# Kernel tuning notes

Measured on AMD Instinct MI355X. Metric: run time of the kernel, lower is better.

## Reference

```python
import jax, jax.numpy as jnp
import numpy as np

B, S, H = 128, 512, 768      # batch, seq, encoder hidden
NL = 42                      # len(LABEL_TO_ID)
LD = 300                     # label_dim
DK, DV = 64, 768             # K_dim, V_dim
HID = 768                    # opt['hidden_dim']
P = 512                      # max_seq_length == pos_indicator
INF = 1e12                   # constant.INFINITY_NUMBER
NEG = -1e9


def gelu(x):
    return 0.5 * x * (1.0 + jax.lax.erf(x * 0.7071067811865476))


def setup_inputs() -> dict:
    key = jax.random.key(0)
    ks = jax.random.split(key, 24)
    sc = 0.02
    return {
        "inputs": jax.random.normal(ks[0], (B, S, H), jnp.float32),
        "pos_ids": jax.random.randint(ks[1], (B, S), 0, 53),
        "dep_ids": jax.random.randint(ks[2], (B, S), 0, 42),
        "subj_pos": jax.random.randint(ks[3], (B, S), 0, P + 1),
        "obj_pos": jax.random.randint(ks[4], (B, S), 0, P + 1),
        "adj": jnp.zeros((1, 1, 1), jnp.float32),  # unused by forward
        # stacked per-label Q/K projections (41 = NL-1 labels, label 0 excluded)
        "WQ": jax.random.normal(ks[5], (NL - 1, DK, H), jnp.float32) * sc,
        "bQ": jax.random.normal(ks[6], (NL - 1, DK), jnp.float32) * sc,
        "WK": jax.random.normal(ks[7], (NL - 1, DK, LD), jnp.float32) * sc,
        "bK": jax.random.normal(ks[8], (NL - 1, DK), jnp.float32) * sc,
        "WV_w": jax.random.normal(ks[9], (DV, H), jnp.float32) * sc,
        "WV_b": jax.random.normal(ks[10], (DV,), jnp.float32) * sc,
        "Wout_w": jax.random.normal(ks[11], (H, DV), jnp.float32) * sc,
        "Wout_b": jax.random.normal(ks[12], (H,), jnp.float32) * sc,
        "ln_g": jnp.ones((H,), jnp.float32),
        "ln_b": jnp.zeros((H,), jnp.float32),
        "label_emb": jax.random.normal(ks[13], (NL, LD), jnp.float32) * sc,
        "feat_w": jax.random.normal(ks[14], (HID, 3 * H), jnp.float32) * sc,
        "feat_b": jax.random.normal(ks[15], (HID,), jnp.float32) * sc,
        "out_w": jax.random.normal(ks[16], (LD, HID), jnp.float32) * sc,
        "out_b": jax.random.normal(ks[17], (LD,), jnp.float32) * sc,
    }


def reference(inputs, pos_ids, dep_ids, subj_pos, obj_pos, adj,
              WQ, bQ, WK, bK, WV_w, WV_b, Wout_w, Wout_b, ln_g, ln_b,
              label_emb, feat_w, feat_b, out_w, out_b):
    dt = inputs.dtype
    # combined attention mask (bool OR, as torch bool+bool): entity markers + padding
    mask = (subj_pos == P) | (obj_pos == P) | (pos_ids == 0)   # [B,S]

    # --- LabelAttention: 41-loop collapses to one fused projection ---
    lab = label_emb[1:NL]                                      # [41,LD] labels 1..41
    kvec = jnp.einsum('ld,lkd->lk', lab, WK) + bK              # [41,DK] per-label keys
    # scores_sum[b,s] = sum_l (x W_Q_l^T + b_Q_l) . k_l  /sqrt(dk)  + 41*mask*NEG
    w_eff = jnp.einsum('lk,lkh->h', kvec, WQ)                  # [H]
    c = jnp.sum(kvec * bQ)                                     # scalar
    scores = (inputs @ w_eff + c) / 8.0                        # sqrt(DK)=8; [B,S]
    scores = scores + (NL - 1) * mask.astype(dt) * NEG
    attn = jax.nn.softmax(scores, axis=-1)                     # [B,S]

    wv = inputs @ WV_w.T + WV_b                                # [B,S,DV]
    ctx = jnp.einsum('bs,bsd->bd', attn, wv)                   # [B,DV]
    ctx = gelu(ctx @ Wout_w.T + Wout_b)                        # [B,H]
    mu = ctx.mean(-1, keepdims=True)
    var = ((ctx - mu) ** 2).mean(-1, keepdims=True)
    ctx = (ctx - mu) / jnp.sqrt(var + 1e-5) * ln_g + ln_b

    # --- entity max pooling (mask True where NOT part of entity) ---
    sm = (subj_pos != P)[:, :, None]
    om = (obj_pos != P)[:, :, None]
    subj_out = jnp.where(sm, -INF, inputs).max(axis=1)         # [B,H]
    obj_out = jnp.where(om, -INF, inputs).max(axis=1)          # [B,H]

    feats = jnp.concatenate([subj_out, obj_out, ctx], axis=-1)  # [B,3H]
    feats = gelu(feats @ feat_w.T + feat_b)                     # [B,HID]
    feats = gelu(feats @ out_w.T + out_b)                       # [B,LD]

    logits = feats @ label_emb.T                                # [B,42]
    return logits, ctx
```

## Files before the change

kernel.cpp:

```cpp
#include <hip/hip_runtime.h>
#include <math.h>

#define BB 128
#define SS 512
#define HH 768
#define PPOS 512
#define NEGC (-1.0e9f)
#define NINF (-1.0e12f)

#define OFF_KVEC   0
#define OFF_WEFF   2624
#define OFF_C      3392
#define OFF_CAT    0
#define OFF_POOLED 294912
#define OFF_PP     393216
#define OFF_PS     1179648
#define OFF_PO     1966080
#define OFF_PZ     2752512
#define OFF_CTXA   393216
#define OFF_CTXB   491520
#define OFF_F1     589824
#define OFF_F2     688128

__device__ __forceinline__ float gelu_f(float x) {
    return 0.5f * x * (1.0f + erff(x * 0.70710678118654752f));
}
__device__ __forceinline__ float dot4(float4 a, float4 b) {
    return a.x*b.x + a.y*b.y + a.z*b.z + a.w*b.w;
}

template<int K4, int ACT, int MT>
__global__ __launch_bounds__(256) void k_mm(const float* __restrict__ A,
        const float* __restrict__ W, const float* __restrict__ bias,
        float* __restrict__ C, int M, int N) {
    int lane = threadIdx.x & 63;
    int wave = (blockIdx.x * 256 + threadIdx.x) >> 6;
    int ntn = (N + 15) >> 4;
    int m0 = (wave / ntn) * MT;
    if (m0 >= M) return;
    int n0 = ((wave % ntn) << 4) + (lane >> 2);
    int ks = lane & 3;
    bool nvalid = (n0 < N);
    const float4* A4 = (const float4*)A;
    const float4* w_row = (const float4*)W + (size_t)(nvalid ? n0 : 0) * K4;
    const float4* ar = A4 + (size_t)m0 * K4;
    float acc[MT];
    #pragma unroll
    for (int r = 0; r < MT; ++r) acc[r] = 0.f;
    #pragma unroll 4
    for (int j = ks; j < K4; j += 4) {
        float4 wv = w_row[j];
        #pragma unroll
        for (int r = 0; r < MT; ++r) acc[r] += dot4(ar[(size_t)r * K4 + j], wv);
    }
    #pragma unroll
    for (int r = 0; r < MT; ++r) {
        acc[r] += __shfl_xor(acc[r], 1, 64);
        acc[r] += __shfl_xor(acc[r], 2, 64);
    }
    if (ks == 0 && nvalid) {
        float b = bias ? bias[n0] : 0.f;
        #pragma unroll
        for (int r = 0; r < MT; ++r) {
            float v = acc[r] + b;
            if (ACT == 1) v = gelu_f(v);
            C[(size_t)(m0 + r) * N + n0] = v;
        }
    }
}

__global__ __launch_bounds__(256) void k_kvec2(const float* __restrict__ label_emb,
        const float* __restrict__ WK, const float* __restrict__ bK,
        float* __restrict__ ws) {
    if (blockIdx.x < 3) ws[OFF_WEFF + blockIdx.x * 256 + threadIdx.x] = 0.f;
    if (blockIdx.x == 3 && threadIdx.x == 0) ws[OFF_C] = 0.f;
    int lane = threadIdx.x & 63;
    int idx = (blockIdx.x * 256 + threadIdx.x) >> 6;
    int l = idx >> 6;
    const float4* lab4 = (const float4*)(label_emb + (size_t)(l + 1) * 300);
    const float4* wk4  = (const float4*)(WK + (size_t)idx * 300);
    float acc = dot4(lab4[lane], wk4[lane]);
    if (lane < 11) acc += dot4(lab4[64 + lane], wk4[64 + lane]);
    #pragma unroll
    for (int off = 32; off > 0; off >>= 1) acc += __shfl_xor(acc, off, 64);
    if (lane == 0) ws[OFF_KVEC + idx] = acc + bK[idx];
}

__global__ __launch_bounds__(256) void k_weff2(const float* __restrict__ WQ,
        const float* __restrict__ bQ, float* __restrict__ ws) {
    int lane = threadIdx.x & 63;
    int w = (blockIdx.x * 256 + threadIdx.x) >> 6;
    if (w < 492) {
        int jc = w / 12, hg = w % 12;
        int h = hg * 64 + lane;
        const float* wq = WQ + (size_t)(jc * 64) * HH + h;
        const float* kv = ws + OFF_KVEC + jc * 64;
        float acc = 0.f;
        #pragma unroll 8
        for (int j = 0; j < 64; ++j) acc += kv[j] * wq[(size_t)j * HH];
        atomicAdd(&ws[OFF_WEFF + h], acc);
    } else if (w == 492) {
        float acc = 0.f;
        for (int j = lane; j < 2624; j += 64) acc += ws[OFF_KVEC + j] * bQ[j];
        #pragma unroll
        for (int off = 32; off > 0; off >>= 1) acc += __shfl_xor(acc, off, 64);
        if (lane == 0) atomicAdd(&ws[OFF_C], acc);
    }
}

__global__ __launch_bounds__(256) void k_fused(const float* __restrict__ inputs,
        const int* __restrict__ pos_ids, const int* __restrict__ subj_pos,
        const int* __restrict__ obj_pos, float* __restrict__ ws) {
    __shared__ float l_pe[4][768];
    __shared__ float l_sm[4][768];
    __shared__ float l_om[4][768];
    __shared__ float l_z[4];
    __shared__ int l_mask[64];
    int chunk = blockIdx.x, b = blockIdx.y;
    int t = threadIdx.x, wave = t >> 6, lane = t & 63;
    int row0 = b * SS + chunk * 64;
    if (t < 64) {
        int g = row0 + t;
        int sp = subj_pos[g], op = obj_pos[g], pi = pos_ids[g];
        int m = ((sp == PPOS) | (op == PPOS) | (pi == 0)) ? 1 : 0;
        if (sp == PPOS) m |= 2;
        if (op == PPOS) m |= 4;
        l_mask[t] = m;
    }
    const float4* w4 = (const float4*)(ws + OFF_WEFF);
    float c = ws[OFF_C];
    float4 w0 = w4[lane], w1 = w4[64 + lane], w2 = w4[128 + lane];
    __syncthreads();
    const float4* in4 = (const float4*)inputs;
    float4 pe0 = make_float4(0.f, 0.f, 0.f, 0.f);
    float4 pe1 = pe0, pe2 = pe0;
    float4 sm0 = make_float4(NINF, NINF, NINF, NINF);
    float4 sm1 = sm0, sm2 = sm0, om0 = sm0, om1 = sm0, om2 = sm0;
    float z = 0.f;
    int rbase = wave * 16;
    #pragma unroll 4
    for (int r = 0; r < 16; ++r) {
        int s = rbase + r;
        const float4* x4 = in4 + (size_t)(row0 + s) * 192;
        float4 x0 = x4[lane], x1 = x4[64 + lane], x2 = x4[128 + lane];
        float acc = dot4(x0, w0) + dot4(x1, w1) + dot4(x2, w2);
        #pragma unroll
        for (int off = 32; off > 0; off >>= 1) acc += __shfl_xor(acc, off, 64);
        int mk = l_mask[s];
        float e = (mk & 1) ? 0.f : __expf((acc + c) * 0.125f);
        z += e;
        pe0.x += e * x0.x; pe0.y += e * x0.y; pe0.z += e * x0.z; pe0.w += e * x0.w;
        pe1.x += e * x1.x; pe1.y += e * x1.y; pe1.z += e * x1.z; pe1.w += e * x1.w;
        pe2.x += e * x2.x; pe2.y += e * x2.y; pe2.z += e * x2.z; pe2.w += e * x2.w;
        if (mk & 2) {
            sm0.x = fmaxf(sm0.x, x0.x); sm0.y = fmaxf(sm0.y, x0.y);
            sm0.z = fmaxf(sm0.z, x0.z); sm0.w = fmaxf(sm0.w, x0.w);
            sm1.x = fmaxf(sm1.x, x1.x); sm1.y = fmaxf(sm1.y, x1.y);
            sm1.z = fmaxf(sm1.z, x1.z); sm1.w = fmaxf(sm1.w, x1.w);
            sm2.x = fmaxf(sm2.x, x2.x); sm2.y = fmaxf(sm2.y, x2.y);
            sm2.z = fmaxf(sm2.z, x2.z); sm2.w = fmaxf(sm2.w, x2.w);
        }
        if (mk & 4) {
            om0.x = fmaxf(om0.x, x0.x); om0.y = fmaxf(om0.y, x0.y);
            om0.z = fmaxf(om0.z, x0.z); om0.w = fmaxf(om0.w, x0.w);
            om1.x = fmaxf(om1.x, x1.x); om1.y = fmaxf(om1.y, x1.y);
            om1.z = fmaxf(om1.z, x1.z); om1.w = fmaxf(om1.w, x1.w);
            om2.x = fmaxf(om2.x, x2.x); om2.y = fmaxf(om2.y, x2.y);
            om2.z = fmaxf(om2.z, x2.z); om2.w = fmaxf(om2.w, x2.w);
        }
    }
    ((float4*)l_pe[wave])[lane] = pe0;
    ((float4*)l_pe[wave])[64 + lane] = pe1;
    ((float4*)l_pe[wave])[128 + lane] = pe2;
    ((float4*)l_sm[wave])[lane] = sm0;
    ((float4*)l_sm[wave])[64 + lane] = sm1;
    ((float4*)l_sm[wave])[128 + lane] = sm2;
    ((float4*)l_om[wave])[lane] = om0;
    ((float4*)l_om[wave])[64 + lane] = om1;
    ((float4*)l_om[wave])[128 + lane] = om2;
    if (lane == 0) l_z[wave] = z;
    __syncthreads();
    if (t < 192) {
        float4 p = make_float4(0.f, 0.f, 0.f, 0.f);
        float4 s = make_float4(NINF, NINF, NINF, NINF);
        float4 o = s;
        #pragma unroll
        for (int w = 0; w < 4; ++w) {
            float4 vp = ((float4*)l_pe[w])[t];
            float4 vs = ((float4*)l_sm[w])[t];
            float4 vo = ((float4*)l_om[w])[t];
            p.x += vp.x; p.y += vp.y; p.z += vp.z; p.w += vp.w;
            s.x = fmaxf(s.x, vs.x); s.y = fmaxf(s.y, vs.y);
            s.z = fmaxf(s.z, vs.z); s.w = fmaxf(s.w, vs.w);
            o.x = fmaxf(o.x, vo.x); o.y = fmaxf(o.y, vo.y);
            o.z = fmaxf(o.z, vo.z); o.w = fmaxf(o.w, vo.w);
        }
        size_t oo = (size_t)(b * 8 + chunk) * 192 + t;
        ((float4*)(ws + OFF_PP))[oo] = p;
        ((float4*)(ws + OFF_PS))[oo] = s;
        ((float4*)(ws + OFF_PO))[oo] = o;
    }
    if (t == 0) ws[OFF_PZ + b * 8 + chunk] = l_z[0] + l_z[1] + l_z[2] + l_z[3];
}

__global__ void k_reduce(float* __restrict__ ws) {
    int i = blockIdx.x * 256 + threadIdx.x;
    int b = i / HH, h = i - b * HH;
    float p = 0.f, sm = NINF, om = NINF, zt = 0.f;
    #pragma unroll
    for (int j = 0; j < 8; ++j) {
        int o = (b * 8 + j) * HH + h;
        p += ws[OFF_PP + o];
        sm = fmaxf(sm, ws[OFF_PS + o]);
        om = fmaxf(om, ws[OFF_PO + o]);
        zt += ws[OFF_PZ + b * 8 + j];
    }
    ws[OFF_POOLED + i] = p / zt;
    ws[OFF_CAT + (size_t)b * 2304 + h] = sm;
    ws[OFF_CAT + (size_t)b * 2304 + 768 + h] = om;
}

__global__ void k_ln(const float* __restrict__ ln_g, const float* __restrict__ ln_b,
                     float* __restrict__ ws, float* __restrict__ out) {
    __shared__ float red[256];
    __shared__ float red2[256];
    int b = blockIdx.x, t = threadIdx.x;
    const float* x = ws + OFF_CTXB + (size_t)b * HH;
    float a0 = x[t], a1 = x[t + 256], a2 = x[t + 512];
    red[t]  = a0 + a1 + a2;
    red2[t] = a0 * a0 + a1 * a1 + a2 * a2;
    __syncthreads();
    for (int s2 = 128; s2 > 0; s2 >>= 1) {
        if (t < s2) { red[t] += red[t + s2]; red2[t] += red2[t + s2]; }
        __syncthreads();
    }
    float mu  = red[0] * (1.0f / 768.0f);
    float var = red2[0] * (1.0f / 768.0f) - mu * mu;
    float inv = rsqrtf(var + 1e-5f);
    float* o = out + 5376 + (size_t)b * HH;
    float* cc = ws + OFF_CAT + (size_t)b * 2304 + 1536;
    float r0 = (a0 - mu) * inv * ln_g[t]       + ln_b[t];
    float r1 = (a1 - mu) * inv * ln_g[t + 256] + ln_b[t + 256];
    float r2 = (a2 - mu) * inv * ln_g[t + 512] + ln_b[t + 512];
    o[t] = r0; o[t + 256] = r1; o[t + 512] = r2;
    cc[t] = r0; cc[t + 256] = r1; cc[t + 512] = r2;
}

extern "C" void kernel_launch(void* const* d_in, const int* in_sizes, int n_in,
                              void* d_out, int out_size, void* d_ws, size_t ws_size,
                              hipStream_t stream) {
    const float* inputs    = (const float*)d_in[0];
    const int*   pos_ids   = (const int*)d_in[1];
    const int*   subj_pos  = (const int*)d_in[3];
    const int*   obj_pos   = (const int*)d_in[4];
    const float* WQ        = (const float*)d_in[6];
    const float* bQ        = (const float*)d_in[7];
    const float* WK        = (const float*)d_in[8];
    const float* bK        = (const float*)d_in[9];
    const float* WV_w      = (const float*)d_in[10];
    const float* WV_b      = (const float*)d_in[11];
    const float* Wout_w    = (const float*)d_in[12];
    const float* Wout_b    = (const float*)d_in[13];
    const float* ln_g      = (const float*)d_in[14];
    const float* ln_b      = (const float*)d_in[15];
    const float* label_emb = (const float*)d_in[16];
    const float* feat_w    = (const float*)d_in[17];
    const float* feat_b    = (const float*)d_in[18];
    const float* out_w     = (const float*)d_in[19];
    const float* out_b     = (const float*)d_in[20];
    float* out = (float*)d_out;
    float* ws  = (float*)d_ws;

    k_kvec2  <<<656, 256, 0, stream>>>(label_emb, WK, bK, ws);
    k_weff2  <<<124, 256, 0, stream>>>(WQ, bQ, ws);
    k_fused  <<<dim3(8, BB), 256, 0, stream>>>(inputs, pos_ids, subj_pos, obj_pos, ws);
    k_reduce <<<384, 256, 0, stream>>>(ws);
    k_mm<192,0,2><<<768, 256, 0, stream>>>(ws + OFF_POOLED, WV_w, WV_b, ws + OFF_CTXA, BB, HH);
    k_mm<192,1,2><<<768, 256, 0, stream>>>(ws + OFF_CTXA, Wout_w, Wout_b, ws + OFF_CTXB, BB, HH);
    k_ln     <<<BB, 256, 0, stream>>>(ln_g, ln_b, ws, out);
    k_mm<576,1,2><<<768, 256, 0, stream>>>(ws + OFF_CAT, feat_w, feat_b, ws + OFF_F1, BB, HH);
    k_mm<192,1,2><<<304, 256, 0, stream>>>(ws + OFF_F1, out_w, out_b, ws + OFF_F2, BB, 300);
    k_mm<75,0,2><<<48, 256, 0, stream>>>(ws + OFF_F2, label_emb, nullptr, out, BB, 42);
}
```

Before: 454.4 us.

## Stage weight tiles in LDS for dense GEMMs and fuse final two layers

The small-M matmul kernel is rewritten so each block loads a 16-row weight tile into shared memory in 64-float4 chunks, and its four waves share that tile across 8 batch rows. The output projection and the label-embedding product are fused into one per-batch tail kernel that keeps the intermediate in shared memory. The aim is to cut redundant global weight reads and one kernel launch, at the cost of extra barriers and a tail kernel that re-reads out_w once per batch row.

Result: slower. 469.4 us (+3.3%).

```diff
diff --git a/kernel.cpp b/kernel.cpp
--- a/kernel.cpp
+++ b/kernel.cpp
@@ -20,7 +20,6 @@
 #define OFF_CTXA   393216
 #define OFF_CTXB   491520
 #define OFF_F1     589824
-#define OFF_F2     688128
 
 __device__ __forceinline__ float gelu_f(float x) {
     return 0.5f * x * (1.0f + erff(x * 0.70710678118654752f));
@@ -29,43 +28,46 @@
     return a.x*b.x + a.y*b.y + a.z*b.z + a.w*b.w;
 }
 
-template<int K4, int ACT, int MT>
-__global__ __launch_bounds__(256) void k_mm(const float* __restrict__ A,
+template<int K4, int ACT>
+__global__ __launch_bounds__(256) void k_mmL(const float* __restrict__ A,
         const float* __restrict__ W, const float* __restrict__ bias,
         float* __restrict__ C, int M, int N) {
-    int lane = threadIdx.x & 63;
-    int wave = (blockIdx.x * 256 + threadIdx.x) >> 6;
-    int ntn = (N + 15) >> 4;
-    int m0 = (wave / ntn) * MT;
-    if (m0 >= M) return;
-    int n0 = ((wave % ntn) << 4) + (lane >> 2);
-    int ks = lane & 3;
-    bool nvalid = (n0 < N);
-    const float4* A4 = (const float4*)A;
-    const float4* w_row = (const float4*)W + (size_t)(nvalid ? n0 : 0) * K4;
-    const float4* ar = A4 + (size_t)m0 * K4;
-    float acc[MT];
-    #pragma unroll
-    for (int r = 0; r < MT; ++r) acc[r] = 0.f;
-    #pragma unroll 4
-    for (int j = ks; j < K4; j += 4) {
-        float4 wv = w_row[j];
+    __shared__ float4 lw[16 * 65];
+    int t = threadIdx.x, lane = t & 63, wave = t >> 6;
+    int ntn = N >> 4;
+    int bm = blockIdx.x / ntn;
+    int bn = blockIdx.x - bm * ntn;
+    int m0 = bm * 8 + wave * 2;
+    int n_sub = lane >> 2, ks = lane & 3;
+    int n0 = (bn << 4) + n_sub;
+    const float4* A4 = (const float4*)A + (size_t)m0 * K4;
+    const float4* Wb = (const float4*)W;
+    float acc0 = 0.f, acc1 = 0.f;
+    for (int c0 = 0; c0 < K4; c0 += 64) {
+        __syncthreads();
         #pragma unroll
-        for (int r = 0; r < MT; ++r) acc[r] += dot4(ar[(size_t)r * K4 + j], wv);
-    }
-    #pragma unroll
-    for (int r = 0; r < MT; ++r) {
-        acc[r] += __shfl_xor(acc[r], 1, 64);
-        acc[r] += __shfl_xor(acc[r], 2, 64);
-    }
-    if (ks == 0 && nvalid) {
+        for (int i = 0; i < 4; ++i) {
+            int li = t * 4 + i;
+            int r = li >> 6, j = li & 63;
+            lw[r * 65 + j] = Wb[(size_t)((bn << 4) + r) * K4 + c0 + j];
+        }
+        __syncthreads();
+        const float4* lrow = lw + n_sub * 65;
+        #pragma unroll 4
+        for (int j = ks; j < 64; j += 4) {
+            float4 wv = lrow[j];
+            acc0 += dot4(A4[c0 + j], wv);
+            acc1 += dot4(A4[K4 + c0 + j], wv);
+        }
+    }
+    acc0 += __shfl_xor(acc0, 1, 64); acc0 += __shfl_xor(acc0, 2, 64);
+    acc1 += __shfl_xor(acc1, 1, 64); acc1 += __shfl_xor(acc1, 2, 64);
+    if (ks == 0) {
         float b = bias ? bias[n0] : 0.f;
-        #pragma unroll
-        for (int r = 0; r < MT; ++r) {
-            float v = acc[r] + b;
-            if (ACT == 1) v = gelu_f(v);
-            C[(size_t)(m0 + r) * N + n0] = v;
-        }
+        float v0 = acc0 + b, v1 = acc1 + b;
+        if (ACT == 1) { v0 = gelu_f(v0); v1 = gelu_f(v1); }
+        C[(size_t)m0 * N + n0] = v0;
+        C[(size_t)(m0 + 1) * N + n0] = v1;
     }
 }
 
@@ -246,6 +248,36 @@
     cc[t] = r0; cc[t + 256] = r1; cc[t + 512] = r2;
 }
 
+__global__ __launch_bounds__(256) void k_tail(const float* __restrict__ F1,
+        const float* __restrict__ out_w, const float* __restrict__ out_b,
+        const float* __restrict__ label_emb, float* __restrict__ out) {
+    __shared__ float f2s[304];
+    int b = blockIdx.x, t = threadIdx.x, lane = t & 63, wave = t >> 6;
+    const float4* A4 = (const float4*)(F1 + (size_t)b * HH);
+    int n_sub = lane >> 2, ks = lane & 3;
+    for (int nt = wave; nt < 19; nt += 4) {
+        int n0 = nt * 16 + n_sub;
+        int nr = (n0 < 300) ? n0 : 299;
+        const float4* w_row = (const float4*)out_w + (size_t)nr * 192;
+        float acc = 0.f;
+        #pragma unroll 4
+        for (int j = ks; j < 192; j += 4) acc += dot4(A4[j], w_row[j]);
+        acc += __shfl_xor(acc, 1, 64);
+        acc += __shfl_xor(acc, 2, 64);
+        if (ks == 0 && n0 < 300) f2s[n0] = gelu_f(acc + out_b[n0]);
+    }
+    __syncthreads();
+    if (t < 168) {
+        int n = t >> 2, k4 = t & 3;
+        const float* le = label_emb + (size_t)n * 300;
+        float acc = 0.f;
+        for (int k = k4; k < 300; k += 4) acc += f2s[k] * le[k];
+        acc += __shfl_xor(acc, 1, 64);
+        acc += __shfl_xor(acc, 2, 64);
+        if (k4 == 0) out[(size_t)b * 42 + n] = acc;
+    }
+}
+
 extern "C" void kernel_launch(void* const* d_in, const int* in_sizes, int n_in,
                               void* d_out, int out_size, void* d_ws, size_t ws_size,
                               hipStream_t stream) {
@@ -275,10 +307,9 @@
     k_weff2  <<<124, 256, 0, stream>>>(WQ, bQ, ws);
     k_fused  <<<dim3(8, BB), 256, 0, stream>>>(inputs, pos_ids, subj_pos, obj_pos, ws);
     k_reduce <<<384, 256, 0, stream>>>(ws);
-    k_mm<192,0,2><<<768, 256, 0, stream>>>(ws + OFF_POOLED, WV_w, WV_b, ws + OFF_CTXA, BB, HH);
-    k_mm<192,1,2><<<768, 256, 0, stream>>>(ws + OFF_CTXA, Wout_w, Wout_b, ws + OFF_CTXB, BB, HH);
+    k_mmL<192,0><<<16 * 48, 256, 0, stream>>>(ws + OFF_POOLED, WV_w, WV_b, ws + OFF_CTXA, BB, HH);
+    k_mmL<192,1><<<16 * 48, 256, 0, stream>>>(ws + OFF_CTXA, Wout_w, Wout_b, ws + OFF_CTXB, BB, HH);
     k_ln     <<<BB, 256, 0, stream>>>(ln_g, ln_b, ws, out);
-    k_mm<576,1,2><<<768, 256, 0, stream>>>(ws + OFF_CAT, feat_w, feat_b, ws + OFF_F1, BB, HH);
-    k_mm<192,1,2><<<304, 256, 0, stream>>>(ws + OFF_F1, out_w, out_b, ws + OFF_F2, BB, 300);
-    k_mm<75,0,2><<<48, 256, 0, stream>>>(ws + OFF_F2, label_emb, nullptr, out, BB, 42);
-}
+    k_mmL<576,1><<<16 * 48, 256, 0, stream>>>(ws + OFF_CAT, feat_w, feat_b, ws + OFF_F1, BB, HH);
+    k_tail   <<<BB, 256, 0, stream>>>(ws + OFF_F1, out_w, out_b, label_emb, out);
+}
```
